# Performance work log

Measured on AMD Instinct MI355X. Metric: run time of the kernel, lower is better.

The kernel has to match this reference:

```python
import jax, jax.numpy as jnp
import numpy as np

B, S, D = 16, 1024, 1024
HEADS = 16
DIM_HEAD = D // HEADS  # 64, used only for the softmax scale (no head split in source)
EPS = 1e-6


def setup_inputs() -> dict:
    key = jax.random.key(0)
    ks = jax.random.split(key, 18)
    inp = {}
    names = ['q_real', 'q_imag', 'k_real', 'k_imag', 'v_real', 'v_imag']
    for i, n in enumerate(names):
        inp[n] = jax.random.normal(ks[i], (B, S, D), dtype=jnp.float32)
    wnames = ['Wq_r', 'Wq_i', 'Wk_r', 'Wk_i', 'Wv_r', 'Wv_i']
    for i, n in enumerate(wnames):
        inp[n] = jax.random.normal(ks[6 + i], (D, D), dtype=jnp.float32) * 0.02
        inp['b' + n[1:]] = jax.random.normal(ks[12 + (i % 6)], (D,), dtype=jnp.float32) * 0.02
    inp['a_2'] = jnp.ones((D,), dtype=jnp.float32)
    inp['b_2'] = jnp.ones((D,), dtype=jnp.float32)
    return inp


def reference(q_real, q_imag, k_real, k_imag, v_real, v_imag,
              Wq_r, bq_r, Wq_i, bq_i, Wk_r, bk_r, Wk_i, bk_i,
              Wv_r, bv_r, Wv_i, bv_i, a_2, b_2):
    # torch nn.Linear: y = x @ W.T + b
    qr = q_real @ Wq_r.T + bq_r
    qi = q_imag @ Wq_i.T + bq_i
    kr = k_real @ Wk_r.T + bk_r
    ki = k_imag @ Wk_i.T + bk_i
    vr = v_real @ Wv_r.T + bv_r
    vi = v_imag @ Wv_i.T + bv_i
    # Faithful to source: transpose(-2, 1) on a 3D tensor is a no-op, so the
    # real branch contracts q's feature dim with k's *sequence* dim (S == D).
    scores = (jnp.einsum('bsd,bde->bse', qr, kr)
              + jnp.einsum('bsd,btd->bst', qi, ki)) / jnp.sqrt(jnp.float32(DIM_HEAD))
    attn = jax.nn.softmax(scores, axis=-1)  # [B, S, S]
    out_r = attn @ vr  # [B, S, D]
    out_i = attn @ vi
    z = out_r + 1j * out_i  # complex64
    # Complex LayerNorm: mean/var computed in complex arithmetic (not |.|^2)
    mean = jnp.mean(z, axis=-1, keepdims=True)
    var = jnp.mean((z - mean) ** 2, axis=-1, keepdims=True)
    std = jnp.sqrt(var + EPS)  # complex sqrt
    y = a_2 * ((z - mean) / std) + b_2
    return jnp.stack([y.real, y.imag])  # [2, B, S, D] real view of complex output
```

## Files before the change

kernel.cpp:

```cpp
#include <hip/hip_runtime.h>


#define MB 1048576L

typedef _Float16 h8 __attribute__((ext_vector_type(8)));
typedef _Float16 h4 __attribute__((ext_vector_type(4)));
typedef float f32x16 __attribute__((ext_vector_type(16)));

__device__ __forceinline__ float wave_sum(float x) {
#pragma unroll
  for (int o = 32; o; o >>= 1) x += __shfl_xor(x, o);
  return x;
}
__device__ __forceinline__ float wave_max(float x) {
#pragma unroll
  for (int o = 32; o; o >>= 1) x = fmaxf(x, __shfl_xor(x, o));
  return x;
}

__device__ __forceinline__ void async16(const char* g, char* l) {
  __builtin_amdgcn_global_load_lds(
      (const __attribute__((address_space(1))) unsigned int*)g,
      (__attribute__((address_space(3))) unsigned int*)l, 16, 0, 0);
}

__device__ __forceinline__ void split8(const float* v, h8& hi, h8& lo) {
#pragma unroll
  for (int j = 0; j < 8; ++j) {
    _Float16 h = (_Float16)v[j];
    hi[j] = h;
    lo[j] = (_Float16)(v[j] - (float)h);
  }
}

__global__ void split_pass(const float* __restrict__ in, char* __restrict__ out, long n8) {
  long i = (long)blockIdx.x * blockDim.x + threadIdx.x;
  if (i >= n8) return;
  float v[8];
  const float4* p = (const float4*)(in + i * 8);
  float4 a = p[0], b = p[1];
  v[0] = a.x; v[1] = a.y; v[2] = a.z; v[3] = a.w;
  v[4] = b.x; v[5] = b.y; v[6] = b.z; v[7] = b.w;
  h8 hi, lo;
  split8(v, hi, lo);
  *(h8*)(out + i * 32) = hi;
  *(h8*)(out + i * 32 + 16) = lo;
}

template <int EPI>
__launch_bounds__(512, 2)
__global__ void gemm_sp(const char* __restrict__ A1, const char* __restrict__ B1,
                        const char* __restrict__ A2, const char* __restrict__ B2,
                        int npair, const float* __restrict__ bias,
                        float* __restrict__ Cf, char* __restrict__ Ct,
                        float scale, long zA, long zB, long zC) {
  __shared__ __align__(16) char lds[131072];
  const int tid = threadIdx.x;
  const int w = tid >> 6, lam = tid & 63;
  const int ln31 = lam & 31, half = lam >> 5;
  const int wr = w >> 2, wc = w & 3;
  const int bm0 = blockIdx.y * 256, bn0 = blockIdx.x * 256;
  const long z = blockIdx.z;

  const char* A1z = A1 + z * zA;
  const char* B1z = B1 + z * zB;
  const char* A2z = A2 ? A2 + z * zA : A1z;
  const char* B2z = B2 ? B2 + z * zB : B1z;

  const int stRow = w * 32 + (lam >> 2);
  const int stU = (lam & 3) ^ ((lam >> 3) & 3);
  const long sAo = (long)(bm0 + stRow) * 4096 + stU * 16;
  const long sBo = (long)(bn0 + stRow) * 4096 + stU * 16;

  const int e2 = (ln31 >> 1) & 3;
  const int offH = ((2 * half) ^ e2) * 16;
  const int offL = ((2 * half + 1) ^ e2) * 16;
  const int rA = (wr * 128 + ln31) * 64;
  const int rB = 16384 + (wc * 64 + ln31) * 64;

  const int Nk = npair * 64;
  f32x16 acc[4][2] = {};

  auto STAGE = [&](int tt) {
    const long ko = (long)(tt & 63) * 64;
    char* d = lds + (tt & 3) * 32768 + w * 2048;
    const char* As = ((tt >> 6) ? A2z : A1z) + sAo + ko;
    const char* Bs = ((tt >> 6) ? B2z : B1z) + sBo + ko;
    async16(As, d);
    async16(As + 65536, d + 1024);
    async16(Bs, d + 16384);
    async16(Bs + 65536, d + 17408);
  };

  STAGE(0);
  STAGE(1);
  STAGE(2);
  __builtin_amdgcn_sched_barrier(0);

  for (int t = 0; t < Nk; ++t) {
    const int left = Nk - t;
    if (left > 3) STAGE(t + 3);
    __builtin_amdgcn_sched_barrier(0);
    if (left > 3)
      asm volatile("s_waitcnt vmcnt(12)" ::: "memory");
    else if (left == 3)
      asm volatile("s_waitcnt vmcnt(8)" ::: "memory");
    else if (left == 2)
      asm volatile("s_waitcnt vmcnt(4)" ::: "memory");
    else
      asm volatile("s_waitcnt vmcnt(0)" ::: "memory");
    __builtin_amdgcn_s_barrier();
    __builtin_amdgcn_sched_barrier(0);

    const char* bq = lds + (t & 3) * 32768;
    h8 bh[2], bl[2], ah[4], al[4];
#pragma unroll
    for (int nt = 0; nt < 2; ++nt) {
      bh[nt] = *(const h8*)(bq + rB + nt * 2048 + offH);
      bl[nt] = *(const h8*)(bq + rB + nt * 2048 + offL);
    }
#pragma unroll
    for (int mt = 0; mt < 4; ++mt) {
      ah[mt] = *(const h8*)(bq + rA + mt * 2048 + offH);
      al[mt] = *(const h8*)(bq + rA + mt * 2048 + offL);
    }
    __builtin_amdgcn_s_setprio(1);
#pragma unroll
    for (int mt = 0; mt < 4; ++mt)
#pragma unroll
      for (int nt = 0; nt < 2; ++nt) {
        acc[mt][nt] = __builtin_amdgcn_mfma_f32_32x32x16_f16(ah[mt], bh[nt], acc[mt][nt], 0, 0, 0);
        acc[mt][nt] = __builtin_amdgcn_mfma_f32_32x32x16_f16(ah[mt], bl[nt], acc[mt][nt], 0, 0, 0);
        acc[mt][nt] = __builtin_amdgcn_mfma_f32_32x32x16_f16(al[mt], bh[nt], acc[mt][nt], 0, 0, 0);
      }
    __builtin_amdgcn_s_setprio(0);
    __builtin_amdgcn_sched_barrier(0);
    __builtin_amdgcn_s_barrier();
  }

  const int wm = wr * 128, wn = wc * 64;
  if (EPI == 0) {
    float* C = Cf + z * zC;
#pragma unroll
    for (int nt = 0; nt < 2; ++nt) {
      const int col = bn0 + wn + nt * 32 + ln31;
      const float bv = bias ? bias[col] : 0.0f;
#pragma unroll
      for (int mt = 0; mt < 4; ++mt) {
#pragma unroll
        for (int q = 0; q < 4; ++q) {
#pragma unroll
          for (int i = 0; i < 4; ++i) {
            const int row = bm0 + wm + mt * 32 + q * 8 + half * 4 + i;
            C[(long)row * 1024 + col] = acc[mt][nt][q * 4 + i] * scale + bv;
          }
        }
      }
    }
  } else {
    const long b = bm0 >> 10;
    char* Tb = Ct + b * (4 * MB);
    const int sbase = bm0 & 1023;
#pragma unroll
    for (int nt = 0; nt < 2; ++nt) {
      const int n = bn0 + wn + nt * 32 + ln31;
      const float bv = bias ? bias[n] : 0.0f;
#pragma unroll
      for (int mt = 0; mt < 4; ++mt) {
#pragma unroll
        for (int q = 0; q < 4; ++q) {
          const int sl = sbase + wm + mt * 32 + q * 8 + half * 4;
          h4 hv, lv;
#pragma unroll
          for (int i = 0; i < 4; ++i) {
            float y = acc[mt][nt][q * 4 + i] * scale + bv;
            _Float16 h = (_Float16)y;
            hv[i] = h;
            lv[i] = (_Float16)(y - (float)h);
          }
          char* dst = Tb + (long)n * 4096 + (sl >> 3) * 32 + (sl & 7) * 2;
          *(h4*)dst = hv;
          *(h4*)(dst + 16) = lv;
        }
      }
    }
  }
}

__launch_bounds__(128)
__global__ void softmax_split(const float* __restrict__ S, char* __restrict__ attn) {
  const long row = blockIdx.x;
  const int t = threadIdx.x;
  const float* p = S + row * 1024 + t * 8;
  float4 a = *(const float4*)p, b = *(const float4*)(p + 4);
  float v[8] = {a.x, a.y, a.z, a.w, b.x, b.y, b.z, b.w};
  float m = v[0];
#pragma unroll
  for (int j = 1; j < 8; ++j) m = fmaxf(m, v[j]);
  m = wave_max(m);
  __shared__ float redm[2], reds[2];
  const int wave = t >> 6, lane = t & 63;
  if (lane == 0) redm[wave] = m;
  __syncthreads();
  m = fmaxf(redm[0], redm[1]);
  float s = 0.f;
#pragma unroll
  for (int j = 0; j < 8; ++j) {
    v[j] = __expf(v[j] - m);
    s += v[j];
  }
  s = wave_sum(s);
  if (lane == 0) reds[wave] = s;
  __syncthreads();
  const float inv = 1.0f / (reds[0] + reds[1]);
#pragma unroll
  for (int j = 0; j < 8; ++j) v[j] *= inv;
  h8 hi, lo;
  split8(v, hi, lo);
  char* dst = attn + row * 4096 + t * 32;
  *(h8*)dst = hi;
  *(h8*)(dst + 16) = lo;
}

__launch_bounds__(256)
__global__ void complex_ln(const float* __restrict__ inr, const float* __restrict__ ini,
                           float* __restrict__ outr, float* __restrict__ outi,
                           const float* __restrict__ a2, const float* __restrict__ b2) {
  const long row = blockIdx.x;
  const int tid = threadIdx.x;
  const float* xr = inr + row * 1024;
  const float* xi = ini + row * 1024;
  float4 r4 = *(const float4*)(xr + tid * 4);
  float4 i4 = *(const float4*)(xi + tid * 4);
  float sx = r4.x + r4.y + r4.z + r4.w;
  float sy = i4.x + i4.y + i4.z + i4.w;
  float sxx = r4.x * r4.x + r4.y * r4.y + r4.z * r4.z + r4.w * r4.w;
  float syy = i4.x * i4.x + i4.y * i4.y + i4.z * i4.z + i4.w * i4.w;
  float sxy = r4.x * i4.x + r4.y * i4.y + r4.z * i4.z + r4.w * i4.w;
  sx = wave_sum(sx); sy = wave_sum(sy);
  sxx = wave_sum(sxx); syy = wave_sum(syy); sxy = wave_sum(sxy);
  __shared__ float red[4][5];
  const int wave = tid >> 6, lane = tid & 63;
  if (lane == 0) {
    red[wave][0] = sx; red[wave][1] = sy; red[wave][2] = sxx;
    red[wave][3] = syy; red[wave][4] = sxy;
  }
  __syncthreads();
  sx = red[0][0] + red[1][0] + red[2][0] + red[3][0];
  sy = red[0][1] + red[1][1] + red[2][1] + red[3][1];
  sxx = red[0][2] + red[1][2] + red[2][2] + red[3][2];
  syy = red[0][3] + red[1][3] + red[2][3] + red[3][3];
  sxy = red[0][4] + red[1][4] + red[2][4] + red[3][4];
  const float invN = 1.0f / 1024.0f;
  const float mx = sx * invN, my = sy * invN;
  const float vx = (sxx * invN - mx * mx) - (syy * invN - my * my);
  const float vy = 2.0f * (sxy * invN - mx * my);
  const float wx = vx + 1e-6f, wy = vy;
  const float rm = sqrtf(wx * wx + wy * wy);
  const float sre = sqrtf(fmaxf(rm + wx, 0.0f) * 0.5f);
  const float sim = copysignf(sqrtf(fmaxf(rm - wx, 0.0f) * 0.5f), wy);
  const float ir = 1.0f / fmaxf(rm, 1e-30f);
  float4 a4 = *(const float4*)(a2 + tid * 4);
  float4 b4 = *(const float4*)(b2 + tid * 4);
  float4 orr, oii;
  {
    float zx = r4.x - mx, zy = i4.x - my;
    orr.x = a4.x * ((zx * sre + zy * sim) * ir) + b4.x;
    oii.x = a4.x * ((zy * sre - zx * sim) * ir);
  }
  {
    float zx = r4.y - mx, zy = i4.y - my;
    orr.y = a4.y * ((zx * sre + zy * sim) * ir) + b4.y;
    oii.y = a4.y * ((zy * sre - zx * sim) * ir);
  }
  {
    float zx = r4.z - mx, zy = i4.z - my;
    orr.z = a4.z * ((zx * sre + zy * sim) * ir) + b4.z;
    oii.z = a4.z * ((zy * sre - zx * sim) * ir);
  }
  {
    float zx = r4.w - mx, zy = i4.w - my;
    orr.w = a4.w * ((zx * sre + zy * sim) * ir) + b4.w;
    oii.w = a4.w * ((zy * sre - zx * sim) * ir);
  }
  *(float4*)(outr + row * 1024 + tid * 4) = orr;
  *(float4*)(outi + row * 1024 + tid * 4) = oii;
}

extern "C" void kernel_launch(void* const* d_in, const int* in_sizes, int n_in,
                              void* d_out, int out_size, void* d_ws, size_t ws_size,
                              hipStream_t stream) {
  const float* X[6];
  for (int i = 0; i < 6; ++i) X[i] = (const float*)d_in[i];
  const float* W[6];
  const float* bia[6];
  for (int i = 0; i < 6; ++i) {
    W[i] = (const float*)d_in[6 + 2 * i];
    bia[i] = (const float*)d_in[7 + 2 * i];
  }
  const float* a2 = (const float*)d_in[18];
  const float* b2 = (const float*)d_in[19];

  char* ws = (char*)d_ws;
  char* qr = ws;
  char* qi = ws + 64 * MB;
  char* ki = ws + 128 * MB;
  char* krT = ws + 192 * MB;
  char* vrT = ws + 256 * MB;
  char* viT = ws + 320 * MB;
  char* Wsp[6];
  for (int i = 0; i < 6; ++i) Wsp[i] = ws + 384 * MB + (long)i * 4 * MB;

  char* dob = (char*)d_out;
  char* Xsp = dob;
  float* F0 = (float*)(dob + 64 * MB);
  float* Sf = (float*)dob;
  char* attn = dob + 64 * MB;
  float* outr = (float*)ws;
  float* outi = (float*)(ws + 64 * MB);

  dim3 blk(256), gblk(512);
  dim3 proj_g(4, 64, 1), bat_g(4, 4, 16);

  for (int i = 0; i < 6; ++i)
    split_pass<<<dim3(512), blk, 0, stream>>>(W[i], Wsp[i], 131072L);

  split_pass<<<dim3(8192), blk, 0, stream>>>(X[0], Xsp, 2097152L);
  gemm_sp<0><<<proj_g, gblk, 0, stream>>>(Xsp, Wsp[0], nullptr, nullptr, 1, bia[0], F0, nullptr, 1.0f, 0, 0, 0);
  split_pass<<<dim3(8192), blk, 0, stream>>>(F0, qr, 2097152L);
  split_pass<<<dim3(8192), blk, 0, stream>>>(X[1], Xsp, 2097152L);
  gemm_sp<0><<<proj_g, gblk, 0, stream>>>(Xsp, Wsp[1], nullptr, nullptr, 1, bia[1], F0, nullptr, 1.0f, 0, 0, 0);
  split_pass<<<dim3(8192), blk, 0, stream>>>(F0, qi, 2097152L);
  split_pass<<<dim3(8192), blk, 0, stream>>>(X[3], Xsp, 2097152L);
  gemm_sp<0><<<proj_g, gblk, 0, stream>>>(Xsp, Wsp[3], nullptr, nullptr, 1, bia[3], F0, nullptr, 1.0f, 0, 0, 0);
  split_pass<<<dim3(8192), blk, 0, stream>>>(F0, ki, 2097152L);
  split_pass<<<dim3(8192), blk, 0, stream>>>(X[2], Xsp, 2097152L);
  gemm_sp<1><<<proj_g, gblk, 0, stream>>>(Xsp, Wsp[2], nullptr, nullptr, 1, bia[2], nullptr, krT, 1.0f, 0, 0, 0);
  split_pass<<<dim3(8192), blk, 0, stream>>>(X[4], Xsp, 2097152L);
  gemm_sp<1><<<proj_g, gblk, 0, stream>>>(Xsp, Wsp[4], nullptr, nullptr, 1, bia[4], nullptr, vrT, 1.0f, 0, 0, 0);
  split_pass<<<dim3(8192), blk, 0, stream>>>(X[5], Xsp, 2097152L);
  gemm_sp<1><<<proj_g, gblk, 0, stream>>>(Xsp, Wsp[5], nullptr, nullptr, 1, bia[5], nullptr, viT, 1.0f, 0, 0, 0);

  gemm_sp<0><<<bat_g, gblk, 0, stream>>>(qr, krT, qi, ki, 2, nullptr, Sf, nullptr, 0.125f,
                                         4 * MB, 4 * MB, 1048576L);
  softmax_split<<<dim3(16384), dim3(128), 0, stream>>>(Sf, attn);
  gemm_sp<0><<<bat_g, gblk, 0, stream>>>(attn, vrT, nullptr, nullptr, 1, nullptr, outr, nullptr, 1.0f,
                                         4 * MB, 4 * MB, 1048576L);
  gemm_sp<0><<<bat_g, gblk, 0, stream>>>(attn, viT, nullptr, nullptr, 1, nullptr, outi, nullptr, 1.0f,
                                         4 * MB, 4 * MB, 1048576L);
  complex_ln<<<dim3(16384), blk, 0, stream>>>(outr, outi, (float*)d_out,
                                              (float*)(dob + 64 * MB), a2, b2);
}
```

Measured before the change: 1.700 ms.

## Double-buffer LDS fragment reads in split-fp16 GEMM and fuse projection split epilogue

Restructures the GEMM main loop to unroll by two, prefetching the next k-tile's LDS fragments into a second register set while MFMAs consume the current set, and drops one barrier per iteration. It also adds an EPI==2 epilogue that transposes the tile through LDS and writes fp16 hi/lo split output directly. This removes the fp32 intermediate write and the separate split_pass for the q_r, q_i and k_i projections. The cost is more live registers from the doubled fragment sets and a bit of extra LDS traffic in the epilogue.

```diff
diff --git a/kernel.cpp b/kernel.cpp
--- a/kernel.cpp
+++ b/kernel.cpp
@@ -92,28 +92,11 @@
     async16(Bs + 65536, d + 17408);
   };
 
-  STAGE(0);
-  STAGE(1);
-  STAGE(2);
-  __builtin_amdgcn_sched_barrier(0);
-
-  for (int t = 0; t < Nk; ++t) {
-    const int left = Nk - t;
-    if (left > 3) STAGE(t + 3);
-    __builtin_amdgcn_sched_barrier(0);
-    if (left > 3)
-      asm volatile("s_waitcnt vmcnt(12)" ::: "memory");
-    else if (left == 3)
-      asm volatile("s_waitcnt vmcnt(8)" ::: "memory");
-    else if (left == 2)
-      asm volatile("s_waitcnt vmcnt(4)" ::: "memory");
-    else
-      asm volatile("s_waitcnt vmcnt(0)" ::: "memory");
-    __builtin_amdgcn_s_barrier();
-    __builtin_amdgcn_sched_barrier(0);
-
-    const char* bq = lds + (t & 3) * 32768;
-    h8 bh[2], bl[2], ah[4], al[4];
+  h8 ahA[4], alA[4], bhA[2], blA[2];
+  h8 ahB[4], alB[4], bhB[2], blB[2];
+
+  auto READF = [&](int tt, h8* ah, h8* al, h8* bh, h8* bl) {
+    const char* bq = lds + (tt & 3) * 32768;
 #pragma unroll
     for (int nt = 0; nt < 2; ++nt) {
       bh[nt] = *(const h8*)(bq + rB + nt * 2048 + offH);
@@ -124,6 +107,9 @@
       ah[mt] = *(const h8*)(bq + rA + mt * 2048 + offH);
       al[mt] = *(const h8*)(bq + rA + mt * 2048 + offL);
     }
+  };
+
+  auto MFMAS = [&](const h8* ah, const h8* al, const h8* bh, const h8* bl) {
     __builtin_amdgcn_s_setprio(1);
 #pragma unroll
     for (int mt = 0; mt < 4; ++mt)
@@ -134,8 +120,43 @@
         acc[mt][nt] = __builtin_amdgcn_mfma_f32_32x32x16_f16(al[mt], bh[nt], acc[mt][nt], 0, 0, 0);
       }
     __builtin_amdgcn_s_setprio(0);
+  };
+
+  STAGE(0);
+  STAGE(1);
+  STAGE(2);
+  asm volatile("s_waitcnt vmcnt(8)" ::: "memory");
+  __builtin_amdgcn_s_barrier();
+  __builtin_amdgcn_sched_barrier(0);
+  READF(0, ahA, alA, bhA, blA);
+
+  for (int t = 0; t < Nk; t += 2) {
+    if (t < Nk - 2)
+      asm volatile("s_waitcnt vmcnt(4)" ::: "memory");
+    else
+      asm volatile("s_waitcnt vmcnt(0)" ::: "memory");
+    __builtin_amdgcn_s_barrier();
     __builtin_amdgcn_sched_barrier(0);
-    __builtin_amdgcn_s_barrier();
+    if (t + 3 < Nk) STAGE(t + 3);
+    READF(t + 1, ahB, alB, bhB, blB);
+    __builtin_amdgcn_sched_barrier(0);
+    MFMAS(ahA, alA, bhA, blA);
+    __builtin_amdgcn_sched_barrier(0);
+
+    const int t1 = t + 1;
+    if (t1 < Nk - 1) {
+      if (t1 < Nk - 2)
+        asm volatile("s_waitcnt vmcnt(4)" ::: "memory");
+      else
+        asm volatile("s_waitcnt vmcnt(0)" ::: "memory");
+      __builtin_amdgcn_s_barrier();
+      __builtin_amdgcn_sched_barrier(0);
+      if (t1 + 3 < Nk) STAGE(t1 + 3);
+      READF(t1 + 1, ahA, alA, bhA, blA);
+    }
+    __builtin_amdgcn_sched_barrier(0);
+    MFMAS(ahB, alB, bhB, blB);
+    __builtin_amdgcn_sched_barrier(0);
   }
 
   const int wm = wr * 128, wn = wc * 64;
@@ -157,7 +178,7 @@
         }
       }
     }
-  } else {
+  } else if (EPI == 1) {
     const long b = bm0 >> 10;
     char* Tb = Ct + b * (4 * MB);
     const int sbase = bm0 & 1023;
@@ -182,6 +203,43 @@
           *(h4*)dst = hv;
           *(h4*)(dst + 16) = lv;
         }
+      }
+    }
+  } else {
+    __syncthreads();
+    float* T = (float*)(lds + w * 8320);
+    const long gr0 = bm0 + wm;
+    const int u0 = (bn0 + wn) >> 3;
+    float bvv[2];
+#pragma unroll
+    for (int nt = 0; nt < 2; ++nt)
+      bvv[nt] = bias ? bias[bn0 + wn + nt * 32 + ln31] : 0.0f;
+    const int r = lam & 31;
+    const int uh = lam >> 5;
+#pragma unroll
+    for (int mt = 0; mt < 4; ++mt) {
+#pragma unroll
+      for (int nt = 0; nt < 2; ++nt) {
+        const int col = nt * 32 + ln31;
+#pragma unroll
+        for (int q = 0; q < 4; ++q) {
+#pragma unroll
+          for (int i = 0; i < 4; ++i)
+            T[(q * 8 + half * 4 + i) * 65 + col] = acc[mt][nt][q * 4 + i] * scale + bvv[nt];
+        }
+      }
+#pragma unroll
+      for (int u4 = 0; u4 < 4; ++u4) {
+        const int u = uh * 4 + u4;
+        const float* src = T + r * 65 + u * 8;
+        float vv[8];
+#pragma unroll
+        for (int j = 0; j < 8; ++j) vv[j] = src[j];
+        h8 hi, lo;
+        split8(vv, hi, lo);
+        char* dst = Ct + (gr0 + mt * 32 + r) * 4096L + (long)(u0 + u) * 32;
+        *(h8*)dst = hi;
+        *(h8*)(dst + 16) = lo;
       }
     }
   }
@@ -313,7 +371,6 @@
 
   char* dob = (char*)d_out;
   char* Xsp = dob;
-  float* F0 = (float*)(dob + 64 * MB);
   float* Sf = (float*)dob;
   char* attn = dob + 64 * MB;
   float* outr = (float*)ws;
@@ -326,14 +383,11 @@
     split_pass<<<dim3(512), blk, 0, stream>>>(W[i], Wsp[i], 131072L);
 
   split_pass<<<dim3(8192), blk, 0, stream>>>(X[0], Xsp, 2097152L);
-  gemm_sp<0><<<proj_g, gblk, 0, stream>>>(Xsp, Wsp[0], nullptr, nullptr, 1, bia[0], F0, nullptr, 1.0f, 0, 0, 0);
-  split_pass<<<dim3(8192), blk, 0, stream>>>(F0, qr, 2097152L);
+  gemm_sp<2><<<proj_g, gblk, 0, stream>>>(Xsp, Wsp[0], nullptr, nullptr, 1, bia[0], nullptr, qr, 1.0f, 0, 0, 0);
   split_pass<<<dim3(8192), blk, 0, stream>>>(X[1], Xsp, 2097152L);
-  gemm_sp<0><<<proj_g, gblk, 0, stream>>>(Xsp, Wsp[1], nullptr, nullptr, 1, bia[1], F0, nullptr, 1.0f, 0, 0, 0);
-  split_pass<<<dim3(8192), blk, 0, stream>>>(F0, qi, 2097152L);
+  gemm_sp<2><<<proj_g, gblk, 0, stream>>>(Xsp, Wsp[1], nullptr, nullptr, 1, bia[1], nullptr, qi, 1.0f, 0, 0, 0);
   split_pass<<<dim3(8192), blk, 0, stream>>>(X[3], Xsp, 2097152L);
-  gemm_sp<0><<<proj_g, gblk, 0, stream>>>(Xsp, Wsp[3], nullptr, nullptr, 1, bia[3], F0, nullptr, 1.0f, 0, 0, 0);
-  split_pass<<<dim3(8192), blk, 0, stream>>>(F0, ki, 2097152L);
+  gemm_sp<2><<<proj_g, gblk, 0, stream>>>(Xsp, Wsp[3], nullptr, nullptr, 1, bia[3], nullptr, ki, 1.0f, 0, 0, 0);
   split_pass<<<dim3(8192), blk, 0, stream>>>(X[2], Xsp, 2097152L);
   gemm_sp<1><<<proj_g, gblk, 0, stream>>>(Xsp, Wsp[2], nullptr, nullptr, 1, bia[2], nullptr, krT, 1.0f, 0, 0, 0);
   split_pass<<<dim3(8192), blk, 0, stream>>>(X[4], Xsp, 2097152L);
```

Measured after the change: 1.633 ms. 3.9% less time.
